# Kernel tuning notes

Measured on AMD Instinct MI355X. Metric: run time of the kernel, lower is better.

## Reference

```python
import jax, jax.numpy as jnp
import numpy as np
import math

K = 8
MOMENTUM = 0.999


def _gelu(x):
    c = math.sqrt(2.0 / math.pi)
    return 0.5 * x * (1.0 + jnp.tanh(c * (x + 0.044715 * x ** 3)))


def _normalize(v, eps=1e-12):
    n = jnp.linalg.norm(v, axis=-1, keepdims=True)
    return v / jnp.maximum(n, eps)


def setup_inputs() -> dict:
    key = jax.random.key(0)
    k1, k2 = jax.random.split(key)
    B, T, D = 4, 4096, 2048
    x = jax.random.normal(k1, (B, T, D), dtype=jnp.float32)
    prototypes = _normalize(jax.random.normal(k2, (K, D), dtype=jnp.float32))
    log_tau = jnp.asarray(math.log(2.0), dtype=jnp.float32)
    log_blend = jnp.asarray(math.log(0.3 / 0.7), dtype=jnp.float32)
    return {"x": x, "prototypes": prototypes, "log_tau": log_tau, "log_blend": log_blend}


def reference(x, prototypes, log_tau, log_blend):
    tau = jnp.exp(log_tau)
    alpha = jax.nn.sigmoid(log_blend)
    B, T, D = x.shape
    x_flat = jax.lax.stop_gradient(x.reshape(-1, D))  # [N, D], detached

    P_norm = _normalize(prototypes)                  # [K, D]
    xn = _normalize(x_flat, eps=1e-8)                # [N, D]

    sims = jnp.clip(xn @ P_norm.T, -1.0, 1.0)        # [N, K]
    assignments = jnp.argmax(sims, axis=-1)          # [N]

    # masked per-cluster mean via segment-sum (vectorized over K)
    sums = jax.ops.segment_sum(x_flat, assignments, num_segments=K)       # [K, D]
    counts = jax.ops.segment_sum(jnp.ones((x_flat.shape[0],), x.dtype),
                                 assignments, num_segments=K)             # [K]
    has = (counts > 0)[:, None]
    centroids = jnp.where(has, sums / jnp.maximum(counts, 1.0)[:, None], prototypes)
    new_P = _normalize(centroids)

    P2 = MOMENTUM * prototypes + (1.0 - MOMENTUM) * new_P
    P2n = _normalize(P2, eps=1e-8)

    sims2 = jnp.clip(xn @ P2n.T, -1.0, 1.0)          # [N, K]
    dists = jnp.clip(1.0 - jnp.max(sims2, axis=-1), 0.0, 2.0)
    novelty = (1.0 - jnp.exp(-tau * dists)).reshape(B, T)

    scale = jnp.clip(1.0 - alpha + alpha * novelty[..., None], 0.1, 10.0)
    return _gelu(x * scale)
```

## Files before the change

### kernel.cpp

```cpp
#include <hip/hip_runtime.h>

#define DDIM  2048
#define KC    8
#define TPB_A 32
#define TPB_C 32

typedef float nfloat4 __attribute__((ext_vector_type(4)));
typedef unsigned short ushortv8 __attribute__((ext_vector_type(8)));
typedef unsigned short ushortv4 __attribute__((ext_vector_type(4)));

__device__ __forceinline__ void nt_store4(const float4& v, float* p){
  nfloat4 nv; nv.x = v.x; nv.y = v.y; nv.z = v.z; nv.w = v.w;
  __builtin_nontemporal_store(nv, (nfloat4*)p);
}
__device__ __forceinline__ void nt_store_us4(const ushortv4& v, unsigned short* p){
  __builtin_nontemporal_store(v, (ushortv4*)p);
}
__device__ __forceinline__ ushortv8 nt_load_us8(const unsigned short* p){
  return __builtin_nontemporal_load((const ushortv8*)p);
}

__device__ __forceinline__ unsigned short f2bf(float f){
  unsigned u = __float_as_uint(f);
  u += 0x7fffu + ((u >> 16) & 1u);
  return (unsigned short)(u >> 16);
}
__device__ __forceinline__ float bf2f(unsigned short h){
  return __uint_as_float(((unsigned)h) << 16);
}
__device__ __forceinline__ float bflo(unsigned u){ return __uint_as_float(u << 16); }
__device__ __forceinline__ float bfhi(unsigned u){ return __uint_as_float(u & 0xffff0000u); }

__device__ __forceinline__ float wave_sum(float v){
  #pragma unroll
  for (int off = 32; off > 0; off >>= 1)
    v += __shfl_xor(v, off, 64);
  return v;
}

__device__ __forceinline__ float butterfly8(float v[8], int t){
  {
    const bool h = (t & 1);
    #pragma unroll
    for (int j = 0; j < 4; ++j){
      float s    = h ? v[j]   : v[j+4];
      float keep = h ? v[j+4] : v[j];
      v[j] = keep + __shfl_xor(s, 1, 64);
    }
  }
  {
    const bool h = (t & 2);
    #pragma unroll
    for (int j = 0; j < 2; ++j){
      float s    = h ? v[j]   : v[j+2];
      float keep = h ? v[j+2] : v[j];
      v[j] = keep + __shfl_xor(s, 2, 64);
    }
  }
  {
    const bool h = (t & 4);
    float s    = h ? v[0] : v[1];
    float keep = h ? v[1] : v[0];
    v[0] = keep + __shfl_xor(s, 4, 64);
  }
  v[0] += __shfl_xor(v[0], 8, 64);
  v[0] += __shfl_xor(v[0], 16, 64);
  v[0] += __shfl_xor(v[0], 32, 64);
  return v[0];
}

__device__ __forceinline__ float gelu_tanh(float v){
  const float c = 0.7978845608028654f;
  float tt = c * v * (1.0f + 0.044715f * v * v);
  float e  = __expf(2.0f * tt);
  float th = 1.0f - 2.0f / (e + 1.0f);
  return 0.5f * v * (1.0f + th);
}

__global__ __launch_bounds__(256, 4)
void k_assign(const float* __restrict__ x, const float* __restrict__ proto,
              unsigned short* __restrict__ part, float* __restrict__ pcnts, int ntok)
{
  __shared__ unsigned short Pl[KC*DDIM];
  __shared__ float rednorm[4*KC];
  __shared__ float sInv[KC];
  __shared__ int   asg[TPB_A];

  const int t = threadIdx.x;
  const int wave = t >> 6, lane = t & 63;
  const int d0 = 4*t, d1 = 1024 + 4*t;

  {
    float4 Q0[KC], Q1[KC];
    #pragma unroll
    for (int k = 0; k < KC; ++k){
      Q0[k] = *(const float4*)(proto + k*DDIM + d0);
      Q1[k] = *(const float4*)(proto + k*DDIM + d1);
    }
    #pragma unroll
    for (int k = 0; k < KC; ++k){
      float ss = Q0[k].x*Q0[k].x + Q0[k].y*Q0[k].y + Q0[k].z*Q0[k].z + Q0[k].w*Q0[k].w
               + Q1[k].x*Q1[k].x + Q1[k].y*Q1[k].y + Q1[k].z*Q1[k].z + Q1[k].w*Q1[k].w;
      ss = wave_sum(ss);
      if (lane == 0) rednorm[wave*KC + k] = ss;
    }
    __syncthreads();
    if (t < KC){
      float ss = rednorm[t] + rednorm[KC+t] + rednorm[2*KC+t] + rednorm[3*KC+t];
      sInv[t] = 1.0f / fmaxf(sqrtf(ss), 1e-12f);
    }
    __syncthreads();
    #pragma unroll
    for (int k = 0; k < KC; ++k){
      const float inv = sInv[k];
      ushortv4 o0, o1;
      o0[0]=f2bf(Q0[k].x*inv); o0[1]=f2bf(Q0[k].y*inv); o0[2]=f2bf(Q0[k].z*inv); o0[3]=f2bf(Q0[k].w*inv);
      o1[0]=f2bf(Q1[k].x*inv); o1[1]=f2bf(Q1[k].y*inv); o1[2]=f2bf(Q1[k].z*inv); o1[3]=f2bf(Q1[k].w*inv);
      *(ushortv4*)(Pl + k*DDIM + d0) = o0;
      *(ushortv4*)(Pl + k*DDIM + d1) = o1;
    }
  }
  __syncthreads();

  const int tok_base = blockIdx.x * TPB_A;

  {
    const int tl0 = wave*8;
    float4 X[8], N[8];
    {
      const int tok = tok_base + tl0;
      if (tok < ntok){
        #pragma unroll
        for (int j = 0; j < 8; ++j)
          X[j] = *(const float4*)(x + (size_t)tok*DDIM + j*256 + 4*lane);
      }
    }
    #pragma unroll
    for (int i = 0; i < 8; ++i){
      const int tok_i = tok_base + tl0 + i;
      const bool ldn = (i < 7) && (tok_i + 1 < ntok);
      if (ldn){
        #pragma unroll
        for (int j = 0; j < 8; ++j)
          N[j] = *(const float4*)(x + (size_t)(tok_i+1)*DDIM + j*256 + 4*lane);
      }
      if (tok_i < ntok){
        float v[KC];
        #pragma unroll
        for (int k = 0; k < KC; ++k){
          float s = 0.f;
          #pragma unroll
          for (int j = 0; j < 8; ++j){
            uint2 u = *(const uint2*)((const unsigned*)Pl + k*1024 + j*128 + 2*lane);
            s += X[j].x*bflo(u.x) + X[j].y*bfhi(u.x)
               + X[j].z*bflo(u.y) + X[j].w*bfhi(u.y);
          }
          v[k] = s;
        }
        float bv = butterfly8(v, lane);
        int   bi = ((lane&1)<<2) | (lane&2) | ((lane>>2)&1);
        #pragma unroll
        for (int off = 1; off < 8; off <<= 1){
          float ov = __shfl_xor(bv, off, 64);
          int   oi = __shfl_xor(bi, off, 64);
          if (ov > bv || (ov == bv && oi < bi)){ bv = ov; bi = oi; }
        }
        if (lane == 0) asg[tl0 + i] = bi;
      }
      if (ldn){
        #pragma unroll
        for (int j = 0; j < 8; ++j) X[j] = N[j];
      }
    }
  }
  __syncthreads();

  float4 acc0[KC], acc1[KC];
  float cnt[KC];
  #pragma unroll
  for (int k = 0; k < KC; ++k){
    acc0[k] = make_float4(0.f,0.f,0.f,0.f);
    acc1[k] = make_float4(0.f,0.f,0.f,0.f);
    cnt[k] = 0.f;
  }
  #pragma unroll
  for (int i = 0; i < TPB_A; ++i){
    const int tok = tok_base + i;
    if (tok < ntok){
      const int a = __builtin_amdgcn_readfirstlane(asg[i]);
      float4 xa = *(const float4*)(x + (size_t)tok*DDIM + d0);
      float4 xb = *(const float4*)(x + (size_t)tok*DDIM + d1);
      #pragma unroll
      for (int k = 0; k < KC; ++k){
        if (a == k){
          acc0[k].x += xa.x; acc0[k].y += xa.y; acc0[k].z += xa.z; acc0[k].w += xa.w;
          acc1[k].x += xb.x; acc1[k].y += xb.y; acc1[k].z += xb.z; acc1[k].w += xb.w;
          cnt[k] += 1.f;
        }
      }
    }
  }
  unsigned short* dst = part + (size_t)blockIdx.x * (KC*DDIM);
  #pragma unroll
  for (int k = 0; k < KC; ++k){
    ushortv4 o0, o1;
    o0[0]=f2bf(acc0[k].x); o0[1]=f2bf(acc0[k].y); o0[2]=f2bf(acc0[k].z); o0[3]=f2bf(acc0[k].w);
    o1[0]=f2bf(acc1[k].x); o1[1]=f2bf(acc1[k].y); o1[2]=f2bf(acc1[k].z); o1[3]=f2bf(acc1[k].w);
    nt_store_us4(o0, dst + k*DDIM + d0);
    nt_store_us4(o1, dst + k*DDIM + d1);
  }
  if (t == 0){
    #pragma unroll
    for (int k = 0; k < KC; ++k) pcnts[blockIdx.x*KC + k] = cnt[k];
  }
}

__global__ __launch_bounds__(256)
void k_reduce(const unsigned short* __restrict__ part, const float* __restrict__ pcnts,
              float* __restrict__ csum, float* __restrict__ ccnt, int nbA)
{
  const int k = blockIdx.x >> 4;
  const int s = blockIdx.x & 15;
  const int t = threadIdx.x;
  const int slot = t & 15;
  const int grp  = t >> 4;

  __shared__ float cmb[16][16][8];
  __shared__ float credn[4];

  const size_t ebase = (size_t)k*DDIM + s*128 + slot*8;
  float a[8] = {0.f,0.f,0.f,0.f,0.f,0.f,0.f,0.f};
  for (int b = grp; b < nbA; b += 16){
    ushortv8 v = nt_load_us8(part + (size_t)b*(KC*DDIM) + ebase);
    #pragma unroll
    for (int j = 0; j < 8; ++j) a[j] += bf2f(v[j]);
  }
  #pragma unroll
  for (int j = 0; j < 8; ++j) cmb[grp][slot][j] = a[j];

  float c = 0.f;
  if (s == 0){
    if (t < nbA)        c += pcnts[t*KC + k];
    if (t + 256 < nbA)  c += pcnts[(t+256)*KC + k];
    c = wave_sum(c);
    if ((t & 63) == 0) credn[t >> 6] = c;
  }
  __syncthreads();

  if (t < 128){
    const int slot2 = t >> 3, j = t & 7;
    float sum = 0.f;
    #pragma unroll
    for (int g = 0; g < 16; ++g) sum += cmb[g][slot2][j];
    csum[(size_t)k*DDIM + s*128 + slot2*8 + j] = sum;
  }
  if (s == 0 && t == 0)
    ccnt[k] = credn[0] + credn[1] + credn[2] + credn[3];
}

__global__ __launch_bounds__(256)
void k_mid(const float* __restrict__ csum, const float* __restrict__ ccnt,
           const float* __restrict__ proto, unsigned short* __restrict__ p2nbf)
{
  const int k = blockIdx.x, t = threadIdx.x;
  const int wave = t >> 6, lane = t & 63;
  __shared__ float s1[4], s2[4];
  const int d0 = 4*t, d1 = 1024 + 4*t;

  float4 a = *(const float4*)(csum + k*DDIM + d0);
  float4 b = *(const float4*)(csum + k*DDIM + d1);
  const float c = ccnt[k];

  float4 pr0 = *(const float4*)(proto + k*DDIM + d0);
  float4 pr1 = *(const float4*)(proto + k*DDIM + d1);

  float4 c0, c1;
  if (c > 0.f){
    const float inv = 1.0f / fmaxf(c, 1.0f);
    c0.x=a.x*inv; c0.y=a.y*inv; c0.z=a.z*inv; c0.w=a.w*inv;
    c1.x=b.x*inv; c1.y=b.y*inv; c1.z=b.z*inv; c1.w=b.w*inv;
  } else { c0 = pr0; c1 = pr1; }

  float ss = c0.x*c0.x + c0.y*c0.y + c0.z*c0.z + c0.w*c0.w
           + c1.x*c1.x + c1.y*c1.y + c1.z*c1.z + c1.w*c1.w;
  ss = wave_sum(ss);
  if (lane == 0) s1[wave] = ss;
  __syncthreads();
  ss = s1[0] + s1[1] + s1[2] + s1[3];
  const float invc = 1.0f / fmaxf(sqrtf(ss), 1e-12f);

  const float m = 0.999f, om = 1.0f - 0.999f;
  float4 p20, p21;
  p20.x = m*pr0.x + om*c0.x*invc; p20.y = m*pr0.y + om*c0.y*invc;
  p20.z = m*pr0.z + om*c0.z*invc; p20.w = m*pr0.w + om*c0.w*invc;
  p21.x = m*pr1.x + om*c1.x*invc; p21.y = m*pr1.y + om*c1.y*invc;
  p21.z = m*pr1.z + om*c1.z*invc; p21.w = m*pr1.w + om*c1.w*invc;

  float ss2 = p20.x*p20.x + p20.y*p20.y + p20.z*p20.z + p20.w*p20.w
            + p21.x*p21.x + p21.y*p21.y + p21.z*p21.z + p21.w*p21.w;
  ss2 = wave_sum(ss2);
  if (lane == 0) s2[wave] = ss2;
  __syncthreads();
  ss2 = s2[0] + s2[1] + s2[2] + s2[3];
  const float inv2 = 1.0f / fmaxf(sqrtf(ss2), 1e-8f);

  ushortv4 o0, o1;
  o0[0]=f2bf(p20.x*inv2); o0[1]=f2bf(p20.y*inv2); o0[2]=f2bf(p20.z*inv2); o0[3]=f2bf(p20.w*inv2);
  o1[0]=f2bf(p21.x*inv2); o1[1]=f2bf(p21.y*inv2); o1[2]=f2bf(p21.z*inv2); o1[3]=f2bf(p21.w*inv2);
  *(ushortv4*)(p2nbf + k*DDIM + d0) = o0;
  *(ushortv4*)(p2nbf + k*DDIM + d1) = o1;
}

__global__ __launch_bounds__(256, 4)
void k_final(const float* __restrict__ x, const unsigned short* __restrict__ p2nbf,
             const float* __restrict__ plt, const float* __restrict__ plb,
             float* __restrict__ out, int ntok)
{
  __shared__ unsigned short Pl[KC*DDIM];
  const int t = threadIdx.x;
  const int wave = t >> 6, lane = t & 63;

  #pragma unroll
  for (int j = 0; j < 8; ++j){
    const int e = (j*256 + t)*8;
    *(ushortv8*)(Pl + e) = *(const ushortv8*)(p2nbf + e);
  }
  __syncthreads();

  const float tau   = __expf(plt[0]);
  const float alpha = 1.0f / (1.0f + __expf(-plb[0]));

  const int tl0 = wave*8;
  const int tok_base = blockIdx.x * TPB_C;
  float4 X[8], N[8];
  {
    const int tok = tok_base + tl0;
    if (tok < ntok){
      #pragma unroll
      for (int j = 0; j < 8; ++j)
        X[j] = *(const float4*)(x + (size_t)tok*DDIM + j*256 + 4*lane);
    }
  }
  #pragma unroll
  for (int i = 0; i < 8; ++i){
    const int tok_i = tok_base + tl0 + i;
    const bool ldn = (i < 7) && (tok_i + 1 < ntok);
    if (ldn){
      #pragma unroll
      for (int j = 0; j < 8; ++j)
        N[j] = *(const float4*)(x + (size_t)(tok_i+1)*DDIM + j*256 + 4*lane);
    }
    if (tok_i < ntok){
      float ss = 0.f;
      #pragma unroll
      for (int j = 0; j < 8; ++j)
        ss += X[j].x*X[j].x + X[j].y*X[j].y + X[j].z*X[j].z + X[j].w*X[j].w;
      ss = wave_sum(ss);

      float v[KC];
      #pragma unroll
      for (int k = 0; k < KC; ++k){
        float s = 0.f;
        #pragma unroll
        for (int j = 0; j < 8; ++j){
          uint2 u = *(const uint2*)((const unsigned*)Pl + k*1024 + j*128 + 2*lane);
          s += X[j].x*bflo(u.x) + X[j].y*bfhi(u.x)
             + X[j].z*bflo(u.y) + X[j].w*bfhi(u.y);
        }
        v[k] = s;
      }
      float mx = butterfly8(v, lane);
      mx = fmaxf(mx, __shfl_xor(mx, 1, 64));
      mx = fmaxf(mx, __shfl_xor(mx, 2, 64));
      mx = fmaxf(mx, __shfl_xor(mx, 4, 64));

      const float inv  = 1.0f / fmaxf(sqrtf(ss), 1e-8f);
      const float s    = fminf(fmaxf(mx * inv, -1.0f), 1.0f);
      const float dist = fminf(fmaxf(1.0f - s, 0.0f), 2.0f);
      const float nov  = 1.0f - __expf(-tau * dist);
      float sc = 1.0f - alpha + alpha * nov;
      sc = fminf(fmaxf(sc, 0.1f), 10.0f);

      float* o = out + (size_t)tok_i*DDIM;
      #pragma unroll
      for (int j = 0; j < 8; ++j){
        float4 g;
        g.x = gelu_tanh(X[j].x*sc); g.y = gelu_tanh(X[j].y*sc);
        g.z = gelu_tanh(X[j].z*sc); g.w = gelu_tanh(X[j].w*sc);
        nt_store4(g, o + j*256 + 4*lane);
      }
    }
    if (ldn){
      #pragma unroll
      for (int j = 0; j < 8; ++j) X[j] = N[j];
    }
  }
}

extern "C" void kernel_launch(void* const* d_in, const int* in_sizes, int n_in,
                              void* d_out, int out_size, void* d_ws, size_t ws_size,
                              hipStream_t stream)
{
  const float* x         = (const float*)d_in[0];
  const float* proto     = (const float*)d_in[1];
  const float* log_tau   = (const float*)d_in[2];
  const float* log_blend = (const float*)d_in[3];
  float* out = (float*)d_out;
  float* ws  = (float*)d_ws;

  const int ntok = in_sizes[0] / DDIM;

  unsigned short* p2nbf = (unsigned short*)(ws);
  float*          pcnts = ws + 8192;
  float*          csum  = ws + 12288;
  float*          ccnt  = ws + 28672;
  unsigned short* part  = (unsigned short*)(ws + 28688);

  const int nbA = (ntok + TPB_A - 1) / TPB_A;
  const int nbC = (ntok + TPB_C - 1) / TPB_C;

  k_assign<<<nbA, 256, 0, stream>>>(x, proto, part, pcnts, ntok);
  k_reduce<<<128, 256, 0, stream>>>(part, pcnts, csum, ccnt, nbA);
  k_mid   <<<KC,  256, 0, stream>>>(csum, ccnt, proto, p2nbf);
  k_final <<<nbC, 256, 0, stream>>>(x, p2nbf, log_tau, log_blend, out, ntok);
}
```

Before: 333.4 us.

## Halve tokens per block and process token pairs sharing prototype LDS reads

Cuts tokens per block from 32 to 16, which doubles the block count for the assign and final kernels. Each wave now handles two tokens at a time, so each bf16 prototype LDS load and its unpacking serve both dot products, replacing the previous one-token software prefetch. The reduce kernel is rescaled to 256 blocks to match the larger number of partial sums, and workspace offsets are moved accordingly. The trade-off is more partial-sum traffic and repeated per-block LDS prototype setup, plus higher register pressure from holding two tokens.

After: 973.5 us. 2.92x slower.

```diff
diff --git a/kernel.cpp b/kernel.cpp
--- a/kernel.cpp
+++ b/kernel.cpp
@@ -2,8 +2,8 @@
 
 #define DDIM  2048
 #define KC    8
-#define TPB_A 32
-#define TPB_C 32
+#define TPB_A 16
+#define TPB_C 16
 
 typedef float nfloat4 __attribute__((ext_vector_type(4)));
 typedef unsigned short ushortv8 __attribute__((ext_vector_type(8)));
@@ -67,6 +67,17 @@
   v[0] += __shfl_xor(v[0], 16, 64);
   v[0] += __shfl_xor(v[0], 32, 64);
   return v[0];
+}
+
+__device__ __forceinline__ int argmax8(float bv, int lane){
+  int bi = ((lane&1)<<2) | (lane&2) | ((lane>>2)&1);
+  #pragma unroll
+  for (int off = 1; off < 8; off <<= 1){
+    float ov = __shfl_xor(bv, off, 64);
+    int   oi = __shfl_xor(bi, off, 64);
+    if (ov > bv || (ov == bv && oi < bi)){ bv = ov; bi = oi; }
+  }
+  return bi;
 }
 
 __device__ __forceinline__ float gelu_tanh(float v){
@@ -125,51 +136,42 @@
   const int tok_base = blockIdx.x * TPB_A;
 
   {
-    const int tl0 = wave*8;
-    float4 X[8], N[8];
-    {
-      const int tok = tok_base + tl0;
-      if (tok < ntok){
+    const int tl0 = wave*4;
+    #pragma unroll
+    for (int p = 0; p < 2; ++p){
+      const int tokA = tok_base + tl0 + 2*p;
+      const int tokB = tokA + 1;
+      const bool vA = tokA < ntok, vB = tokB < ntok;
+      float4 XA[8], XB[8];
+      #pragma unroll
+      for (int j = 0; j < 8; ++j){
+        XA[j] = vA ? *(const float4*)(x + (size_t)tokA*DDIM + j*256 + 4*lane)
+                   : make_float4(0,0,0,0);
+        XB[j] = vB ? *(const float4*)(x + (size_t)tokB*DDIM + j*256 + 4*lane)
+                   : make_float4(0,0,0,0);
+      }
+      float va[KC], vb[KC];
+      #pragma unroll
+      for (int k = 0; k < KC; ++k){
+        float sA = 0.f, sB = 0.f;
         #pragma unroll
-        for (int j = 0; j < 8; ++j)
-          X[j] = *(const float4*)(x + (size_t)tok*DDIM + j*256 + 4*lane);
-      }
-    }
-    #pragma unroll
-    for (int i = 0; i < 8; ++i){
-      const int tok_i = tok_base + tl0 + i;
-      const bool ldn = (i < 7) && (tok_i + 1 < ntok);
-      if (ldn){
-        #pragma unroll
-        for (int j = 0; j < 8; ++j)
-          N[j] = *(const float4*)(x + (size_t)(tok_i+1)*DDIM + j*256 + 4*lane);
-      }
-      if (tok_i < ntok){
-        float v[KC];
-        #pragma unroll
-        for (int k = 0; k < KC; ++k){
-          float s = 0.f;
-          #pragma unroll
-          for (int j = 0; j < 8; ++j){
-            uint2 u = *(const uint2*)((const unsigned*)Pl + k*1024 + j*128 + 2*lane);
-            s += X[j].x*bflo(u.x) + X[j].y*bfhi(u.x)
-               + X[j].z*bflo(u.y) + X[j].w*bfhi(u.y);
-          }
-          v[k] = s;
+        for (int j = 0; j < 8; ++j){
+          uint2 u = *(const uint2*)((const unsigned*)Pl + k*1024 + j*128 + 2*lane);
+          const float p0 = bflo(u.x), p1 = bfhi(u.x), p2 = bflo(u.y), p3 = bfhi(u.y);
+          sA += XA[j].x*p0 + XA[j].y*p1 + XA[j].z*p2 + XA[j].w*p3;
+          sB += XB[j].x*p0 + XB[j].y*p1 + XB[j].z*p2 + XB[j].w*p3;
         }
-        float bv = butterfly8(v, lane);
-        int   bi = ((lane&1)<<2) | (lane&2) | ((lane>>2)&1);
-        #pragma unroll
-        for (int off = 1; off < 8; off <<= 1){
-          float ov = __shfl_xor(bv, off, 64);
-          int   oi = __shfl_xor(bi, off, 64);
-          if (ov > bv || (ov == bv && oi < bi)){ bv = ov; bi = oi; }
-        }
-        if (lane == 0) asg[tl0 + i] = bi;
-      }
-      if (ldn){
-        #pragma unroll
-        for (int j = 0; j < 8; ++j) X[j] = N[j];
+        va[k] = sA; vb[k] = sB;
+      }
+      if (vA){
+        float bv = butterfly8(va, lane);
+        int bi = argmax8(bv, lane);
+        if (lane == 0) asg[tl0 + 2*p] = bi;
+      }
+      if (vB){
+        float bv = butterfly8(vb, lane);
+        int bi = argmax8(bv, lane);
+        if (lane == 0) asg[tl0 + 2*p + 1] = bi;
       }
     }
   }
@@ -219,18 +221,18 @@
 void k_reduce(const unsigned short* __restrict__ part, const float* __restrict__ pcnts,
               float* __restrict__ csum, float* __restrict__ ccnt, int nbA)
 {
-  const int k = blockIdx.x >> 4;
-  const int s = blockIdx.x & 15;
+  const int k = blockIdx.x >> 5;
+  const int s = blockIdx.x & 31;
   const int t = threadIdx.x;
-  const int slot = t & 15;
-  const int grp  = t >> 4;
-
-  __shared__ float cmb[16][16][8];
+  const int slot = t & 7;
+  const int grp  = t >> 3;
+
+  __shared__ float cmb[32][8][8];
   __shared__ float credn[4];
 
-  const size_t ebase = (size_t)k*DDIM + s*128 + slot*8;
+  const size_t ebase = (size_t)k*DDIM + s*64 + slot*8;
   float a[8] = {0.f,0.f,0.f,0.f,0.f,0.f,0.f,0.f};
-  for (int b = grp; b < nbA; b += 16){
+  for (int b = grp; b < nbA; b += 32){
     ushortv8 v = nt_load_us8(part + (size_t)b*(KC*DDIM) + ebase);
     #pragma unroll
     for (int j = 0; j < 8; ++j) a[j] += bf2f(v[j]);
@@ -240,19 +242,18 @@
 
   float c = 0.f;
   if (s == 0){
-    if (t < nbA)        c += pcnts[t*KC + k];
-    if (t + 256 < nbA)  c += pcnts[(t+256)*KC + k];
+    for (int b = t; b < nbA; b += 256) c += pcnts[b*KC + k];
     c = wave_sum(c);
     if ((t & 63) == 0) credn[t >> 6] = c;
   }
   __syncthreads();
 
-  if (t < 128){
+  if (t < 64){
     const int slot2 = t >> 3, j = t & 7;
     float sum = 0.f;
     #pragma unroll
-    for (int g = 0; g < 16; ++g) sum += cmb[g][slot2][j];
-    csum[(size_t)k*DDIM + s*128 + slot2*8 + j] = sum;
+    for (int g = 0; g < 32; ++g) sum += cmb[g][slot2][j];
+    csum[(size_t)k*DDIM + s*64 + slot2*8 + j] = sum;
   }
   if (s == 0 && t == 0)
     ccnt[k] = credn[0] + credn[1] + credn[2] + credn[3];
@@ -330,53 +331,59 @@
   const float tau   = __expf(plt[0]);
   const float alpha = 1.0f / (1.0f + __expf(-plb[0]));
 
-  const int tl0 = wave*8;
+  const int tl0 = wave*4;
   const int tok_base = blockIdx.x * TPB_C;
-  float4 X[8], N[8];
-  {
-    const int tok = tok_base + tl0;
-    if (tok < ntok){
+
+  #pragma unroll
+  for (int p = 0; p < 2; ++p){
+    const int tokA = tok_base + tl0 + 2*p;
+    const int tokB = tokA + 1;
+    const bool vA = tokA < ntok, vB = tokB < ntok;
+    float4 XA[8], XB[8];
+    #pragma unroll
+    for (int j = 0; j < 8; ++j){
+      XA[j] = vA ? *(const float4*)(x + (size_t)tokA*DDIM + j*256 + 4*lane)
+                 : make_float4(0,0,0,0);
+      XB[j] = vB ? *(const float4*)(x + (size_t)tokB*DDIM + j*256 + 4*lane)
+                 : make_float4(0,0,0,0);
+    }
+    float ssA = 0.f, ssB = 0.f;
+    #pragma unroll
+    for (int j = 0; j < 8; ++j){
+      ssA += XA[j].x*XA[j].x + XA[j].y*XA[j].y + XA[j].z*XA[j].z + XA[j].w*XA[j].w;
+      ssB += XB[j].x*XB[j].x + XB[j].y*XB[j].y + XB[j].z*XB[j].z + XB[j].w*XB[j].w;
+    }
+    ssA = wave_sum(ssA);
+    ssB = wave_sum(ssB);
+
+    float va[KC], vb[KC];
+    #pragma unroll
+    for (int k = 0; k < KC; ++k){
+      float sA = 0.f, sB = 0.f;
       #pragma unroll
-      for (int j = 0; j < 8; ++j)
-        X[j] = *(const float4*)(x + (size_t)tok*DDIM + j*256 + 4*lane);
-    }
-  }
-  #pragma unroll
-  for (int i = 0; i < 8; ++i){
-    const int tok_i = tok_base + tl0 + i;
-    const bool ldn = (i < 7) && (tok_i + 1 < ntok);
-    if (ldn){
-      #pragma unroll
-      for (int j = 0; j < 8; ++j)
-        N[j] = *(const float4*)(x + (size_t)(tok_i+1)*DDIM + j*256 + 4*lane);
-    }
-    if (tok_i < ntok){
-      float ss = 0.f;
-      #pragma unroll
-      for (int j = 0; j < 8; ++j)
-        ss += X[j].x*X[j].x + X[j].y*X[j].y + X[j].z*X[j].z + X[j].w*X[j].w;
-      ss = wave_sum(ss);
-
-      float v[KC];
-      #pragma unroll
-      for (int k = 0; k < KC; ++k){
-        float s = 0.f;
-        #pragma unroll
-        for (int j = 0; j < 8; ++j){
-          uint2 u = *(const uint2*)((const unsigned*)Pl + k*1024 + j*128 + 2*lane);
-          s += X[j].x*bflo(u.x) + X[j].y*bfhi(u.x)
-             + X[j].z*bflo(u.y) + X[j].w*bfhi(u.y);
-        }
-        v[k] = s;
-      }
-      float mx = butterfly8(v, lane);
+      for (int j = 0; j < 8; ++j){
+        uint2 u = *(const uint2*)((const unsigned*)Pl + k*1024 + j*128 + 2*lane);
+        const float p0 = bflo(u.x), p1 = bfhi(u.x), p2 = bflo(u.y), p3 = bfhi(u.y);
+        sA += XA[j].x*p0 + XA[j].y*p1 + XA[j].z*p2 + XA[j].w*p3;
+        sB += XB[j].x*p0 + XB[j].y*p1 + XB[j].z*p2 + XB[j].w*p3;
+      }
+      va[k] = sA; vb[k] = sB;
+    }
+
+    #pragma unroll
+    for (int q = 0; q < 2; ++q){
+      const bool vv = q ? vB : vA;
+      if (!vv) continue;
+      const int tok_i = q ? tokB : tokA;
+      float mx = butterfly8(q ? vb : va, lane);
       mx = fmaxf(mx, __shfl_xor(mx, 1, 64));
       mx = fmaxf(mx, __shfl_xor(mx, 2, 64));
       mx = fmaxf(mx, __shfl_xor(mx, 4, 64));
+      const float ss = q ? ssB : ssA;
 
       const float inv  = 1.0f / fmaxf(sqrtf(ss), 1e-8f);
-      const float s    = fminf(fmaxf(mx * inv, -1.0f), 1.0f);
-      const float dist = fminf(fmaxf(1.0f - s, 0.0f), 2.0f);
+      const float sv   = fminf(fmaxf(mx * inv, -1.0f), 1.0f);
+      const float dist = fminf(fmaxf(1.0f - sv, 0.0f), 2.0f);
       const float nov  = 1.0f - __expf(-tau * dist);
       float sc = 1.0f - alpha + alpha * nov;
       sc = fminf(fmaxf(sc, 0.1f), 10.0f);
@@ -384,15 +391,12 @@
       float* o = out + (size_t)tok_i*DDIM;
       #pragma unroll
       for (int j = 0; j < 8; ++j){
+        const float4 Xj = q ? XB[j] : XA[j];
         float4 g;
-        g.x = gelu_tanh(X[j].x*sc); g.y = gelu_tanh(X[j].y*sc);
-        g.z = gelu_tanh(X[j].z*sc); g.w = gelu_tanh(X[j].w*sc);
+        g.x = gelu_tanh(Xj.x*sc); g.y = gelu_tanh(Xj.y*sc);
+        g.z = gelu_tanh(Xj.z*sc); g.w = gelu_tanh(Xj.w*sc);
         nt_store4(g, o + j*256 + 4*lane);
       }
-    }
-    if (ldn){
-      #pragma unroll
-      for (int j = 0; j < 8; ++j) X[j] = N[j];
     }
   }
 }
@@ -412,15 +416,15 @@
 
   unsigned short* p2nbf = (unsigned short*)(ws);
   float*          pcnts = ws + 8192;
-  float*          csum  = ws + 12288;
-  float*          ccnt  = ws + 28672;
-  unsigned short* part  = (unsigned short*)(ws + 28688);
+  float*          csum  = ws + 16384;
+  float*          ccnt  = ws + 32768;
+  unsigned short* part  = (unsigned short*)(ws + 32784);
 
   const int nbA = (ntok + TPB_A - 1) / TPB_A;
   const int nbC = (ntok + TPB_C - 1) / TPB_C;
 
   k_assign<<<nbA, 256, 0, stream>>>(x, proto, part, pcnts, ntok);
-  k_reduce<<<128, 256, 0, stream>>>(part, pcnts, csum, ccnt, nbA);
+  k_reduce<<<256, 256, 0, stream>>>(part, pcnts, csum, ccnt, nbA);
   k_mid   <<<KC,  256, 0, stream>>>(csum, ccnt, proto, p2nbf);
   k_final <<<nbC, 256, 0, stream>>>(x, p2nbf, log_tau, log_blend, out, ntok);
 }
```

## Halve tokens per block, restructure dot loop, widen reduction grid

Applied to the files above, without the earlier changes.

Halves the tokens per block in the assign and final kernels, which doubles the block count for more parallelism. It reorders the prototype dot product so all K LDS loads for a column chunk are issued before the FMAs, and adds sched barriers after the prefetch. The reduction kernel is widened to 256 blocks with 32 groups to handle twice as many partials, and the workspace offsets grow to fit. The cost is twice as many bf16 partial sums written and reduced, plus twice as many prototype LDS fills per token.

Result: no change. 339.1 us (+1.7%).

```diff
diff --git a/kernel.cpp b/kernel.cpp
--- a/kernel.cpp
+++ b/kernel.cpp
@@ -2,8 +2,8 @@
 
 #define DDIM  2048
 #define KC    8
-#define TPB_A 32
-#define TPB_C 32
+#define TPB_A 16
+#define TPB_C 16
 
 typedef float nfloat4 __attribute__((ext_vector_type(4)));
 typedef unsigned short ushortv8 __attribute__((ext_vector_type(8)));
@@ -67,6 +67,17 @@
   v[0] += __shfl_xor(v[0], 16, 64);
   v[0] += __shfl_xor(v[0], 32, 64);
   return v[0];
+}
+
+__device__ __forceinline__ int argmax8(float bv, int lane){
+  int bi = ((lane&1)<<2) | (lane&2) | ((lane>>2)&1);
+  #pragma unroll
+  for (int off = 1; off < 8; off <<= 1){
+    float ov = __shfl_xor(bv, off, 64);
+    int   oi = __shfl_xor(bi, off, 64);
+    if (ov > bv || (ov == bv && oi < bi)){ bv = ov; bi = oi; }
+  }
+  return bi;
 }
 
 __device__ __forceinline__ float gelu_tanh(float v){
@@ -75,6 +86,25 @@
   float e  = __expf(2.0f * tt);
   float th = 1.0f - 2.0f / (e + 1.0f);
   return 0.5f * v * (1.0f + th);
+}
+
+__device__ __forceinline__ void dot8(const unsigned* Pw, const float4 X[8],
+                                     float va[KC], int lane)
+{
+  #pragma unroll
+  for (int k = 0; k < KC; ++k) va[k] = 0.f;
+  #pragma unroll
+  for (int j = 0; j < 8; ++j){
+    uint2 u[KC];
+    #pragma unroll
+    for (int k = 0; k < KC; ++k)
+      u[k] = *(const uint2*)(Pw + k*1024 + j*128 + 2*lane);
+    #pragma unroll
+    for (int k = 0; k < KC; ++k){
+      va[k] += X[j].x*bflo(u[k].x) + X[j].y*bfhi(u[k].x)
+             + X[j].z*bflo(u[k].y) + X[j].w*bfhi(u[k].y);
+    }
+  }
 }
 
 __global__ __launch_bounds__(256, 4)
@@ -123,9 +153,10 @@
   __syncthreads();
 
   const int tok_base = blockIdx.x * TPB_A;
-
-  {
-    const int tl0 = wave*8;
+  const unsigned* Pw = (const unsigned*)Pl;
+
+  {
+    const int tl0 = wave*4;
     float4 X[8], N[8];
     {
       const int tok = tok_base + tl0;
@@ -136,35 +167,20 @@
       }
     }
     #pragma unroll
-    for (int i = 0; i < 8; ++i){
+    for (int i = 0; i < 4; ++i){
       const int tok_i = tok_base + tl0 + i;
-      const bool ldn = (i < 7) && (tok_i + 1 < ntok);
+      const bool ldn = (i < 3) && (tok_i + 1 < ntok);
       if (ldn){
         #pragma unroll
         for (int j = 0; j < 8; ++j)
           N[j] = *(const float4*)(x + (size_t)(tok_i+1)*DDIM + j*256 + 4*lane);
       }
+      __builtin_amdgcn_sched_barrier(0);
       if (tok_i < ntok){
-        float v[KC];
-        #pragma unroll
-        for (int k = 0; k < KC; ++k){
-          float s = 0.f;
-          #pragma unroll
-          for (int j = 0; j < 8; ++j){
-            uint2 u = *(const uint2*)((const unsigned*)Pl + k*1024 + j*128 + 2*lane);
-            s += X[j].x*bflo(u.x) + X[j].y*bfhi(u.x)
-               + X[j].z*bflo(u.y) + X[j].w*bfhi(u.y);
-          }
-          v[k] = s;
-        }
-        float bv = butterfly8(v, lane);
-        int   bi = ((lane&1)<<2) | (lane&2) | ((lane>>2)&1);
-        #pragma unroll
-        for (int off = 1; off < 8; off <<= 1){
-          float ov = __shfl_xor(bv, off, 64);
-          int   oi = __shfl_xor(bi, off, 64);
-          if (ov > bv || (ov == bv && oi < bi)){ bv = ov; bi = oi; }
-        }
+        float va[KC];
+        dot8(Pw, X, va, lane);
+        float bv = butterfly8(va, lane);
+        int bi = argmax8(bv, lane);
         if (lane == 0) asg[tl0 + i] = bi;
       }
       if (ldn){
@@ -219,18 +235,18 @@
 void k_reduce(const unsigned short* __restrict__ part, const float* __restrict__ pcnts,
               float* __restrict__ csum, float* __restrict__ ccnt, int nbA)
 {
-  const int k = blockIdx.x >> 4;
-  const int s = blockIdx.x & 15;
+  const int k = blockIdx.x >> 5;
+  const int s = blockIdx.x & 31;
   const int t = threadIdx.x;
-  const int slot = t & 15;
-  const int grp  = t >> 4;
-
-  __shared__ float cmb[16][16][8];
+  const int slot = t & 7;
+  const int grp  = t >> 3;
+
+  __shared__ float cmb[32][8][8];
   __shared__ float credn[4];
 
-  const size_t ebase = (size_t)k*DDIM + s*128 + slot*8;
+  const size_t ebase = (size_t)k*DDIM + s*64 + slot*8;
   float a[8] = {0.f,0.f,0.f,0.f,0.f,0.f,0.f,0.f};
-  for (int b = grp; b < nbA; b += 16){
+  for (int b = grp; b < nbA; b += 32){
     ushortv8 v = nt_load_us8(part + (size_t)b*(KC*DDIM) + ebase);
     #pragma unroll
     for (int j = 0; j < 8; ++j) a[j] += bf2f(v[j]);
@@ -240,19 +256,18 @@
 
   float c = 0.f;
   if (s == 0){
-    if (t < nbA)        c += pcnts[t*KC + k];
-    if (t + 256 < nbA)  c += pcnts[(t+256)*KC + k];
+    for (int b = t; b < nbA; b += 256) c += pcnts[b*KC + k];
     c = wave_sum(c);
     if ((t & 63) == 0) credn[t >> 6] = c;
   }
   __syncthreads();
 
-  if (t < 128){
+  if (t < 64){
     const int slot2 = t >> 3, j = t & 7;
     float sum = 0.f;
     #pragma unroll
-    for (int g = 0; g < 16; ++g) sum += cmb[g][slot2][j];
-    csum[(size_t)k*DDIM + s*128 + slot2*8 + j] = sum;
+    for (int g = 0; g < 32; ++g) sum += cmb[g][slot2][j];
+    csum[(size_t)k*DDIM + s*64 + slot2*8 + j] = sum;
   }
   if (s == 0 && t == 0)
     ccnt[k] = credn[0] + credn[1] + credn[2] + credn[3];
@@ -330,8 +345,10 @@
   const float tau   = __expf(plt[0]);
   const float alpha = 1.0f / (1.0f + __expf(-plb[0]));
 
-  const int tl0 = wave*8;
+  const int tl0 = wave*4;
   const int tok_base = blockIdx.x * TPB_C;
+  const unsigned* Pw = (const unsigned*)Pl;
+
   float4 X[8], N[8];
   {
     const int tok = tok_base + tl0;
@@ -342,41 +359,33 @@
     }
   }
   #pragma unroll
-  for (int i = 0; i < 8; ++i){
+  for (int i = 0; i < 4; ++i){
     const int tok_i = tok_base + tl0 + i;
-    const bool ldn = (i < 7) && (tok_i + 1 < ntok);
+    const bool ldn = (i < 3) && (tok_i + 1 < ntok);
     if (ldn){
       #pragma unroll
       for (int j = 0; j < 8; ++j)
         N[j] = *(const float4*)(x + (size_t)(tok_i+1)*DDIM + j*256 + 4*lane);
     }
+    __builtin_amdgcn_sched_barrier(0);
     if (tok_i < ntok){
+      float va[KC];
+      dot8(Pw, X, va, lane);
+
       float ss = 0.f;
       #pragma unroll
       for (int j = 0; j < 8; ++j)
         ss += X[j].x*X[j].x + X[j].y*X[j].y + X[j].z*X[j].z + X[j].w*X[j].w;
       ss = wave_sum(ss);
 
-      float v[KC];
-      #pragma unroll
-      for (int k = 0; k < KC; ++k){
-        float s = 0.f;
-        #pragma unroll
-        for (int j = 0; j < 8; ++j){
-          uint2 u = *(const uint2*)((const unsigned*)Pl + k*1024 + j*128 + 2*lane);
-          s += X[j].x*bflo(u.x) + X[j].y*bfhi(u.x)
-             + X[j].z*bflo(u.y) + X[j].w*bfhi(u.y);
-        }
-        v[k] = s;
-      }
-      float mx = butterfly8(v, lane);
+      float mx = butterfly8(va, lane);
       mx = fmaxf(mx, __shfl_xor(mx, 1, 64));
       mx = fmaxf(mx, __shfl_xor(mx, 2, 64));
       mx = fmaxf(mx, __shfl_xor(mx, 4, 64));
 
       const float inv  = 1.0f / fmaxf(sqrtf(ss), 1e-8f);
-      const float s    = fminf(fmaxf(mx * inv, -1.0f), 1.0f);
-      const float dist = fminf(fmaxf(1.0f - s, 0.0f), 2.0f);
+      const float sv   = fminf(fmaxf(mx * inv, -1.0f), 1.0f);
+      const float dist = fminf(fmaxf(1.0f - sv, 0.0f), 2.0f);
       const float nov  = 1.0f - __expf(-tau * dist);
       float sc = 1.0f - alpha + alpha * nov;
       sc = fminf(fmaxf(sc, 0.1f), 10.0f);
@@ -412,15 +421,15 @@
 
   unsigned short* p2nbf = (unsigned short*)(ws);
   float*          pcnts = ws + 8192;
-  float*          csum  = ws + 12288;
-  float*          ccnt  = ws + 28672;
-  unsigned short* part  = (unsigned short*)(ws + 28688);
+  float*          csum  = ws + 16384;
+  float*          ccnt  = ws + 32768;
+  unsigned short* part  = (unsigned short*)(ws + 32784);
 
   const int nbA = (ntok + TPB_A - 1) / TPB_A;
   const int nbC = (ntok + TPB_C - 1) / TPB_C;
 
   k_assign<<<nbA, 256, 0, stream>>>(x, proto, part, pcnts, ntok);
-  k_reduce<<<128, 256, 0, stream>>>(part, pcnts, csum, ccnt, nbA);
+  k_reduce<<<256, 256, 0, stream>>>(part, pcnts, csum, ccnt, nbA);
   k_mid   <<<KC,  256, 0, stream>>>(csum, ccnt, proto, p2nbf);
   k_final <<<nbC, 256, 0, stream>>>(x, p2nbf, log_tau, log_blend, out, ntok);
 }
```
